# Kernel tuning notes

Hardware: AMD Instinct MI355X
Metric: run time of the kernel (lower is better)

The kernel has to match this reference:

```python
import jax, jax.numpy as jnp
import numpy as np

N_NODES = 100000
NINP = 128
N_EDGES = 1600000
EPS = 1e-12


def _gcn_conv(x, W, b, src, dst, deg_inv_sqrt):
    # PyG GCNConv: h = x W; out = D^{-1/2}(A+I)D^{-1/2} h + b
    h = x @ W  # [N, out_dim]
    norm = deg_inv_sqrt[src] * deg_inv_sqrt[dst]  # [E]
    agg = jax.ops.segment_sum(h[src] * norm[:, None], dst, num_segments=N_NODES)
    # self-loop contribution: weight deg_inv_sqrt[i]^2
    agg = agg + h * (deg_inv_sqrt ** 2)[:, None]
    return agg + b


def setup_inputs() -> dict:
    key = jax.random.key(0)
    k1, k2, k3, k4 = jax.random.split(key, 4)
    edge_index = jax.random.randint(k1, (2, N_EDGES), 0, N_NODES, dtype=jnp.int64)
    # embedding table (xavier-normal-like), padding_idx=0 row zeroed
    emb = jax.random.normal(k2, (N_NODES, NINP), dtype=jnp.float32) * (2.0 / (N_NODES + NINP)) ** 0.5
    emb = emb.at[0].set(0.0)
    W1 = jax.random.normal(k3, (NINP, 2 * NINP), dtype=jnp.float32) * (1.0 / NINP) ** 0.5
    b1 = jnp.zeros((2 * NINP,), dtype=jnp.float32)
    W2 = jax.random.normal(k4, (2 * NINP, NINP), dtype=jnp.float32) * (1.0 / (2 * NINP)) ** 0.5
    b2 = jnp.zeros((NINP,), dtype=jnp.float32)
    return {"emb": emb, "W1": W1, "b1": b1, "W2": W2, "b2": b2, "edge_index": edge_index}


def reference(emb, W1, b1, W2, b2, edge_index):
    src, dst = edge_index[0], edge_index[1]
    # symmetric GCN degree with self-loops (in-degree on dst + 1)
    deg = jax.ops.segment_sum(jnp.ones_like(dst, dtype=emb.dtype), dst, num_segments=N_NODES) + 1.0
    deg_inv_sqrt = jax.lax.rsqrt(deg)
    x = _gcn_conv(emb, W1, b1, src, dst, deg_inv_sqrt)  # [N, 2*ninp]
    # F.normalize(p=2, dim=-1)
    x = x / jnp.maximum(jnp.linalg.norm(x, axis=-1, keepdims=True), EPS)
    # dropout in eval mode (identity)
    out = _gcn_conv(x, W2, b2, src, dst, deg_inv_sqrt)  # [N, ninp]
    return out
```

## Files before the change

### kernel.cpp

```cpp
#include <hip/hip_runtime.h>
#include <hip/hip_bf16.h>

typedef __attribute__((ext_vector_type(8))) short bf16x8;
typedef __attribute__((ext_vector_type(4))) float f32x4;

#define NBUCK 391
#define BCAP 8192


__device__ __forceinline__ ushort f2bf(float f) {
    unsigned int b = __float_as_uint(f);
    unsigned int r = (b + 0x7fffu + ((b >> 16) & 1u)) >> 16;
    return (ushort)r;
}
__device__ __forceinline__ float bflo(uint v) { return __uint_as_float(v << 16); }
__device__ __forceinline__ float bfhi(uint v) { return __uint_as_float(v & 0xffff0000u); }


__global__ __launch_bounds__(256) void prep_kernel(const float* __restrict__ W1, ushort* __restrict__ W1t,
                                                   const float* __restrict__ W2, ushort* __restrict__ W2t,
                                                   int* __restrict__ gcur) {
    int b = blockIdx.x, t = threadIdx.x;
    if (b == 0) {
        if (t < NBUCK) gcur[t] = 0;
        if (t + 256 < NBUCK) gcur[t + 256] = 0;
    } else if (b <= 128) {
        int i = (b - 1) * 256 + t;
        int n = i >> 7, k = i & 127;
        W1t[i] = f2bf(W1[(size_t)k * 256 + n]);
    } else {
        int i = (b - 129) * 256 + t;
        int n = i >> 8, k = i & 255;
        W2t[i] = f2bf(W2[(size_t)k * 128 + n]);
    }
}


__global__ __launch_bounds__(256) void bucket_kernel(const int* __restrict__ src, const int* __restrict__ dst,
                                                     int* __restrict__ gcur, int2* __restrict__ pairs,
                                                     int E, int chunk) {
    __shared__ int lcnt[NBUCK];
    for (int t = threadIdx.x; t < NBUCK; t += 256) lcnt[t] = 0;
    __syncthreads();
    int e0 = blockIdx.x * chunk;
    int e1 = e0 + chunk; if (e1 > E) e1 = E;
    for (int e = e0 + (int)threadIdx.x; e < e1; e += 256)
        atomicAdd(&lcnt[dst[e] >> 8], 1);
    __syncthreads();
    for (int t = threadIdx.x; t < NBUCK; t += 256) {
        int c = lcnt[t];
        lcnt[t] = c ? atomicAdd(&gcur[t], c) : 0;
    }
    __syncthreads();
    for (int e = e0 + (int)threadIdx.x; e < e1; e += 256) {
        int d = dst[e], s = src[e];
        int b = d >> 8;
        int p = atomicAdd(&lcnt[b], 1);
        if (p < BCAP) pairs[(size_t)b * BCAP + p] = make_int2(d, s);
    }
}


__global__ __launch_bounds__(512) void scan_buckets(const int* __restrict__ gcur, int* __restrict__ bbase,
                                                    int* __restrict__ offs, int Nn, int E) {
    int i = threadIdx.x;
    int v = (i < NBUCK) ? min(gcur[i], BCAP) : 0;
    int lane = i & 63, wid = i >> 6;
    int x = v;
#pragma unroll
    for (int d = 1; d < 64; d <<= 1) {
        int y = __shfl_up(x, d, 64);
        if (lane >= d) x += y;
    }
    __shared__ int wsum[8], wpre[8];
    if (lane == 63) wsum[wid] = x;
    __syncthreads();
    if (i == 0) {
        int run = 0;
        for (int w = 0; w < 8; ++w) { wpre[w] = run; run += wsum[w]; }
        offs[Nn] = E;
    }
    __syncthreads();
    if (i < NBUCK) bbase[i] = x - v + wpre[wid];
}


__global__ __launch_bounds__(256) void csr_kernel(const int2* __restrict__ pairs, const int* __restrict__ gcur,
                                                  const int* __restrict__ bbase,
                                                  int* __restrict__ offs, float* __restrict__ dis,
                                                  int* __restrict__ csr, int Nn) {
    int b = blockIdx.x;
    int n0 = b << 8;
    int ne = min(gcur[b], BCAP);
    __shared__ int cnt[256], off[256], pos[256];
    int i = threadIdx.x;
    cnt[i] = 0;
    __syncthreads();
    const int2* pp = pairs + (size_t)b * BCAP;
    for (int e = i; e < ne; e += 256)
        atomicAdd(&cnt[pp[e].x - n0], 1);
    __syncthreads();
    int lane = i & 63, wid = i >> 6;
    int v = cnt[i];
    int x = v;
#pragma unroll
    for (int d = 1; d < 64; d <<= 1) {
        int y = __shfl_up(x, d, 64);
        if (lane >= d) x += y;
    }
    __shared__ int wsum[4], wpre[4];
    if (lane == 63) wsum[wid] = x;
    __syncthreads();
    if (i == 0) {
        int run = 0;
        for (int w = 0; w < 4; ++w) { wpre[w] = run; run += wsum[w]; }
    }
    __syncthreads();
    int excl = x - v + wpre[wid];
    off[i] = excl;
    pos[i] = 0;
    int n = n0 + i;
    if (n < Nn) {
        offs[n] = bbase[b] + excl;
        dis[n] = rsqrtf((float)v + 1.0f);
    }
    __syncthreads();
    int base = bbase[b];
    for (int e = i; e < ne; e += 256) {
        int2 r = pp[e];
        int li = r.x - n0;
        int p = atomicAdd(&pos[li], 1);
        csr[base + off[li] + p] = r.y;
    }
}


__global__ void cast_scale_kernel(const float4* __restrict__ in, const float* __restrict__ dis,
                                  ushort4* __restrict__ out, int n4) {
    int stride = gridDim.x * blockDim.x;
    for (int i = blockIdx.x * blockDim.x + threadIdx.x; i < n4; i += stride) {
        float s = dis[i >> 5];
        float4 v = in[i];
        ushort4 o;
        o.x = f2bf(v.x * s); o.y = f2bf(v.y * s); o.z = f2bf(v.z * s); o.w = f2bf(v.w * s);
        out[i] = o;
    }
}


template <bool BIAS, bool BF16OUT>
__global__ __launch_bounds__(256) void agg_kernel(const uint* __restrict__ tbl,
                                                  const int* __restrict__ offs,
                                                  const int* __restrict__ rec,
                                                  const float* __restrict__ dis,
                                                  const float* __restrict__ bias,
                                                  void* __restrict__ outp, int Nn) {
    int gw = (int)((blockIdx.x * 256 + threadIdx.x) >> 6);
    uint lane = threadIdx.x & 63;
    if (gw >= Nn) return;
    float dn = dis[gw];
    int e0 = offs[gw], e1 = offs[gw + 1];
    uint hv = tbl[(uint)gw * 64u + lane];
    float ax = bflo(hv), ay = bfhi(hv);

    for (int base = e0; base < e1; base += 16) {
        int ee = base + (int)(lane & 15u);
        uint rr = (uint)rec[ee < e1 ? ee : e1 - 1];
        uint vv[16];
#pragma unroll
        for (int j = 0; j < 16; ++j) {
            uint idx = (uint)__shfl((int)rr, j, 64);
            vv[j] = tbl[idx * 64u + lane];
        }
#pragma unroll
        for (int j = 0; j < 16; ++j) {
            uint v = (base + j < e1) ? vv[j] : 0u;
            ax += bflo(v);
            ay += bfhi(v);
        }
    }

    ax *= dn; ay *= dn;
    if (BIAS) {
        float2 bv = reinterpret_cast<const float2*>(bias)[lane];
        ax += bv.x; ay += bv.y;
    }
    if (BF16OUT) {
        reinterpret_cast<uint*>(outp)[(uint)gw * 64u + lane] =
            (uint)f2bf(ax) | ((uint)f2bf(ay) << 16);
    } else {
        float2 o; o.x = ax; o.y = ay;
        reinterpret_cast<float2*>(outp)[(uint)gw * 64u + lane] = o;
    }
}


__global__ __launch_bounds__(512, 4) void fused_gemm(const ushort* __restrict__ A,
                                                     const ushort* __restrict__ W1t,
                                                     const float* __restrict__ bias1,
                                                     const ushort* __restrict__ W2t,
                                                     const float* __restrict__ dsc,
                                                     ushort* __restrict__ out2, int M) {
    __shared__ __align__(16) ushort sA[64 * 128];
    __shared__ __align__(16) ushort xt[64 * 256];
    __shared__ float ssl[8][64];
    int tid = threadIdx.x;
    int lane = tid & 63, wid = tid >> 6;
    int g = lane >> 4, i15 = lane & 15;
    int koff = g * 8;
    int m0 = blockIdx.x * 64;

    {
        const char* Ab = reinterpret_cast<const char*>(A);
        char* sAb = reinterpret_cast<char*>(sA);
#pragma unroll
        for (int j = 0; j < 2; ++j) {
            int byte = j * 8192 + tid * 16;
            int row = byte >> 8;
            int grow = m0 + row; if (grow >= M) grow = M - 1;
            bf16x8 v = *reinterpret_cast<const bf16x8*>(Ab + (size_t)grow * 256 + (byte & 255));
            *reinterpret_cast<bf16x8*>(sAb + (byte ^ ((row & 7) << 4))) = v;
        }
    }

    bf16x8 b1f[2][4];
    float bv[2];
#pragma unroll
    for (int ns = 0; ns < 2; ++ns) {
        int c = wid * 32 + ns * 16 + i15;
        const bf16x8* p = reinterpret_cast<const bf16x8*>(W1t + (size_t)c * 128 + koff);
#pragma unroll
        for (int ks = 0; ks < 4; ++ks) b1f[ns][ks] = p[ks * 4];
        bv[ns] = bias1[c];
    }
    __syncthreads();

    const char* sAb = reinterpret_cast<const char*>(sA);
    f32x4 acc[4][2];
#pragma unroll
    for (int ms = 0; ms < 4; ++ms)
#pragma unroll
        for (int ns = 0; ns < 2; ++ns) acc[ms][ns] = (f32x4){0.f, 0.f, 0.f, 0.f};
#pragma unroll
    for (int ks = 0; ks < 4; ++ks) {
        bf16x8 a[4];
#pragma unroll
        for (int ms = 0; ms < 4; ++ms) {
            int row = ms * 16 + i15;
            int byte = row * 256 + ks * 64 + g * 16;
            a[ms] = *reinterpret_cast<const bf16x8*>(sAb + (byte ^ ((row & 7) << 4)));
        }
#pragma unroll
        for (int ms = 0; ms < 4; ++ms)
#pragma unroll
            for (int ns = 0; ns < 2; ++ns)
                acc[ms][ns] = __builtin_amdgcn_mfma_f32_16x16x32_bf16(a[ms], b1f[ns][ks], acc[ms][ns], 0, 0, 0);
    }

    float ps[4][4];
#pragma unroll
    for (int ms = 0; ms < 4; ++ms)
#pragma unroll
        for (int r = 0; r < 4; ++r) {
            float s = 0.f;
#pragma unroll
            for (int ns = 0; ns < 2; ++ns) {
                float v = acc[ms][ns][r] + bv[ns];
                acc[ms][ns][r] = v;
                s += v * v;
            }
            ps[ms][r] = s;
        }
#pragma unroll
    for (int d = 1; d < 16; d <<= 1)
#pragma unroll
        for (int ms = 0; ms < 4; ++ms)
#pragma unroll
            for (int r = 0; r < 4; ++r) ps[ms][r] += __shfl_xor(ps[ms][r], d, 64);
    if (i15 == 0) {
#pragma unroll
        for (int ms = 0; ms < 4; ++ms)
#pragma unroll
            for (int r = 0; r < 4; ++r) ssl[wid][ms * 16 + g * 4 + r] = ps[ms][r];
    }
    __syncthreads();

#pragma unroll
    for (int ms = 0; ms < 4; ++ms)
#pragma unroll
        for (int r = 0; r < 4; ++r) {
            int rt = ms * 16 + g * 4 + r;
            float tot = 0.f;
#pragma unroll
            for (int w = 0; w < 8; ++w) tot += ssl[w][rt];
            float inv = 1.0f / fmaxf(sqrtf(tot), 1e-12f);
            int sw = (rt & 7) << 3;
#pragma unroll
            for (int ns = 0; ns < 2; ++ns) {
                int col = wid * 32 + ns * 16 + i15;
                xt[(rt * 256 + col) ^ sw] = f2bf(acc[ms][ns][r] * inv);
            }
        }
    __syncthreads();

    bf16x8 b2f[8];
    {
        int c = wid * 16 + i15;
        const bf16x8* p = reinterpret_cast<const bf16x8*>(W2t + (size_t)c * 256 + koff);
#pragma unroll
        for (int ks = 0; ks < 8; ++ks) b2f[ks] = p[ks * 4];
    }

    f32x4 acc2[4];
#pragma unroll
    for (int ms = 0; ms < 4; ++ms) acc2[ms] = (f32x4){0.f, 0.f, 0.f, 0.f};
#pragma unroll
    for (int ks = 0; ks < 8; ++ks) {
        bf16x8 a2[4];
#pragma unroll
        for (int ms = 0; ms < 4; ++ms) {
            int rowA = ms * 16 + i15;
            int eb = (rowA * 256 + koff + ks * 32) ^ ((rowA & 7) << 3);
            a2[ms] = *reinterpret_cast<const bf16x8*>(&xt[eb]);
        }
#pragma unroll
        for (int ms = 0; ms < 4; ++ms)
            acc2[ms] = __builtin_amdgcn_mfma_f32_16x16x32_bf16(a2[ms], b2f[ks], acc2[ms], 0, 0, 0);
    }

#pragma unroll
    for (int ms = 0; ms < 4; ++ms)
#pragma unroll
        for (int r = 0; r < 4; ++r) {
            int row = m0 + ms * 16 + g * 4 + r;
            if (row < M) {
                float sc = dsc[row];
                out2[(size_t)row * 128 + wid * 16 + i15] = f2bf(acc2[ms][r] * sc);
            }
        }
}


extern "C" void kernel_launch(void* const* d_in, const int* in_sizes, int n_in,
                              void* d_out, int out_size, void* d_ws, size_t ws_size,
                              hipStream_t stream) {
    const float* emb = (const float*)d_in[0];
    const float* W1 = (const float*)d_in[1];
    const float* b1 = (const float*)d_in[2];
    const float* W2 = (const float*)d_in[3];
    const float* b2 = (const float*)d_in[4];
    const int* eidx = (const int*)d_in[5];

    const int Nn = in_sizes[0] / 128;
    const int E = in_sizes[5] / 2;
    const int* srcp = eidx;
    const int* dstp = eidx + E;

    float* ws = (float*)d_ws;
    size_t o = 0;
    uint* tbl1 = (uint*)(ws + o);  o += (size_t)Nn * 64;
    uint* axb = (uint*)(ws + o);   o += (size_t)Nn * 64;
    uint* tbl2 = (uint*)(ws + o);  o += (size_t)Nn * 64;
    ushort* W1t = (ushort*)(ws + o); o += 128 * 256 / 2;
    ushort* W2t = (ushort*)(ws + o); o += 256 * 128 / 2;
    float* dis = ws + o;    o += Nn;
    int* gcur = (int*)(ws + o);   o += NBUCK + 1;
    int* bbase = (int*)(ws + o);  o += NBUCK + 1;
    int* offs = (int*)(ws + o);   o += Nn + 16;
    int* csr = (int*)(ws + o);    o += E;
    int2* pairs = (int2*)(ws + o); o += (size_t)NBUCK * BCAP * 2;

    prep_kernel<<<257, 256, 0, stream>>>(W1, W1t, W2, W2t, gcur);

    int B1B = 512;
    int chunk = (E + B1B - 1) / B1B;
    bucket_kernel<<<B1B, 256, 0, stream>>>(srcp, dstp, gcur, pairs, E, chunk);
    scan_buckets<<<1, 512, 0, stream>>>(gcur, bbase, offs, Nn, E);
    csr_kernel<<<NBUCK, 256, 0, stream>>>(pairs, gcur, bbase, offs, dis, csr, Nn);

    int n4 = Nn * 128 / 4;
    cast_scale_kernel<<<2048, 256, 0, stream>>>((const float4*)emb, dis, (ushort4*)tbl1, n4);

    agg_kernel<false, true><<<(Nn + 3) / 4, 256, 0, stream>>>(tbl1, offs, csr, dis, nullptr, axb, Nn);
    fused_gemm<<<(Nn + 63) / 64, 512, 0, stream>>>((const ushort*)axb, W1t, b1, W2t, dis, (ushort*)tbl2, Nn);

    agg_kernel<true, false><<<(Nn + 3) / 4, 256, 0, stream>>>(tbl2, offs, csr, dis, b2, d_out, Nn);
}
```

Measured before the change: 234.7 us.

## Fuse prep/cast into bucket and CSR kernels; aggregate two nodes per wave

After: 233.8 us. About the same (-0.4%).

```diff
diff --git a/kernel.cpp b/kernel.cpp
--- a/kernel.cpp
+++ b/kernel.cpp
@@ -17,46 +17,42 @@
 __device__ __forceinline__ float bfhi(uint v) { return __uint_as_float(v & 0xffff0000u); }
 
 
-__global__ __launch_bounds__(256) void prep_kernel(const float* __restrict__ W1, ushort* __restrict__ W1t,
-                                                   const float* __restrict__ W2, ushort* __restrict__ W2t,
-                                                   int* __restrict__ gcur) {
-    int b = blockIdx.x, t = threadIdx.x;
-    if (b == 0) {
-        if (t < NBUCK) gcur[t] = 0;
-        if (t + 256 < NBUCK) gcur[t + 256] = 0;
-    } else if (b <= 128) {
-        int i = (b - 1) * 256 + t;
-        int n = i >> 7, k = i & 127;
-        W1t[i] = f2bf(W1[(size_t)k * 256 + n]);
-    } else {
-        int i = (b - 129) * 256 + t;
-        int n = i >> 8, k = i & 255;
-        W2t[i] = f2bf(W2[(size_t)k * 128 + n]);
-    }
-}
-
-
 __global__ __launch_bounds__(256) void bucket_kernel(const int* __restrict__ src, const int* __restrict__ dst,
                                                      int* __restrict__ gcur, int2* __restrict__ pairs,
-                                                     int E, int chunk) {
+                                                     int E, int chunk,
+                                                     const float* __restrict__ W1, ushort* __restrict__ W1t,
+                                                     const float* __restrict__ W2, ushort* __restrict__ W2t) {
+    int b = blockIdx.x, t = threadIdx.x;
+    if (b >= 512) {
+        if (b < 640) {
+            int i = (b - 512) * 256 + t;
+            int n = i >> 7, k = i & 127;
+            W1t[i] = f2bf(W1[(size_t)k * 256 + n]);
+        } else {
+            int i = (b - 640) * 256 + t;
+            int n = i >> 8, k = i & 255;
+            W2t[i] = f2bf(W2[(size_t)k * 128 + n]);
+        }
+        return;
+    }
     __shared__ int lcnt[NBUCK];
-    for (int t = threadIdx.x; t < NBUCK; t += 256) lcnt[t] = 0;
-    __syncthreads();
-    int e0 = blockIdx.x * chunk;
+    for (int q = t; q < NBUCK; q += 256) lcnt[q] = 0;
+    __syncthreads();
+    int e0 = b * chunk;
     int e1 = e0 + chunk; if (e1 > E) e1 = E;
-    for (int e = e0 + (int)threadIdx.x; e < e1; e += 256)
+    for (int e = e0 + t; e < e1; e += 256)
         atomicAdd(&lcnt[dst[e] >> 8], 1);
     __syncthreads();
-    for (int t = threadIdx.x; t < NBUCK; t += 256) {
-        int c = lcnt[t];
-        lcnt[t] = c ? atomicAdd(&gcur[t], c) : 0;
-    }
-    __syncthreads();
-    for (int e = e0 + (int)threadIdx.x; e < e1; e += 256) {
+    for (int q = t; q < NBUCK; q += 256) {
+        int c = lcnt[q];
+        lcnt[q] = c ? atomicAdd(&gcur[q], c) : 0;
+    }
+    __syncthreads();
+    for (int e = e0 + t; e < e1; e += 256) {
         int d = dst[e], s = src[e];
-        int b = d >> 8;
-        int p = atomicAdd(&lcnt[b], 1);
-        if (p < BCAP) pairs[(size_t)b * BCAP + p] = make_int2(d, s);
+        int bb = d >> 8;
+        int p = atomicAdd(&lcnt[bb], 1);
+        if (p < BCAP) pairs[(size_t)bb * BCAP + p] = make_int2(d, s);
     }
 }
 
@@ -88,11 +84,14 @@
 __global__ __launch_bounds__(256) void csr_kernel(const int2* __restrict__ pairs, const int* __restrict__ gcur,
                                                   const int* __restrict__ bbase,
                                                   int* __restrict__ offs, float* __restrict__ dis,
-                                                  int* __restrict__ csr, int Nn) {
+                                                  int* __restrict__ csr,
+                                                  const float4* __restrict__ emb4, ushort4* __restrict__ tbl4,
+                                                  int Nn) {
     int b = blockIdx.x;
     int n0 = b << 8;
     int ne = min(gcur[b], BCAP);
     __shared__ int cnt[256], off[256], pos[256];
+    __shared__ float sdis[256];
     int i = threadIdx.x;
     cnt[i] = 0;
     __syncthreads();
@@ -120,9 +119,11 @@
     off[i] = excl;
     pos[i] = 0;
     int n = n0 + i;
+    float s = rsqrtf((float)v + 1.0f);
+    sdis[i] = s;
     if (n < Nn) {
         offs[n] = bbase[b] + excl;
-        dis[n] = rsqrtf((float)v + 1.0f);
+        dis[n] = s;
     }
     __syncthreads();
     int base = bbase[b];
@@ -132,65 +133,74 @@
         int p = atomicAdd(&pos[li], 1);
         csr[base + off[li] + p] = r.y;
     }
-}
-
-
-__global__ void cast_scale_kernel(const float4* __restrict__ in, const float* __restrict__ dis,
-                                  ushort4* __restrict__ out, int n4) {
-    int stride = gridDim.x * blockDim.x;
-    for (int i = blockIdx.x * blockDim.x + threadIdx.x; i < n4; i += stride) {
-        float s = dis[i >> 5];
-        float4 v = in[i];
-        ushort4 o;
-        o.x = f2bf(v.x * s); o.y = f2bf(v.y * s); o.z = f2bf(v.z * s); o.w = f2bf(v.w * s);
-        out[i] = o;
+    for (int q = i; q < 256 * 32; q += 256) {
+        int rw = q >> 5;
+        int nn = n0 + rw;
+        if (nn < Nn) {
+            float sc = sdis[rw];
+            float4 vv = emb4[(size_t)nn * 32 + (q & 31)];
+            ushort4 o;
+            o.x = f2bf(vv.x * sc); o.y = f2bf(vv.y * sc);
+            o.z = f2bf(vv.z * sc); o.w = f2bf(vv.w * sc);
+            tbl4[(size_t)nn * 32 + (q & 31)] = o;
+        }
     }
 }
 
 
 template <bool BIAS, bool BF16OUT>
-__global__ __launch_bounds__(256) void agg_kernel(const uint* __restrict__ tbl,
-                                                  const int* __restrict__ offs,
-                                                  const int* __restrict__ rec,
-                                                  const float* __restrict__ dis,
-                                                  const float* __restrict__ bias,
-                                                  void* __restrict__ outp, int Nn) {
-    int gw = (int)((blockIdx.x * 256 + threadIdx.x) >> 6);
-    uint lane = threadIdx.x & 63;
-    if (gw >= Nn) return;
-    float dn = dis[gw];
-    int e0 = offs[gw], e1 = offs[gw + 1];
-    uint hv = tbl[(uint)gw * 64u + lane];
-    float ax = bflo(hv), ay = bfhi(hv);
-
-    for (int base = e0; base < e1; base += 16) {
-        int ee = base + (int)(lane & 15u);
-        uint rr = (uint)rec[ee < e1 ? ee : e1 - 1];
-        uint vv[16];
-#pragma unroll
-        for (int j = 0; j < 16; ++j) {
-            uint idx = (uint)__shfl((int)rr, j, 64);
-            vv[j] = tbl[idx * 64u + lane];
-        }
-#pragma unroll
-        for (int j = 0; j < 16; ++j) {
-            uint v = (base + j < e1) ? vv[j] : 0u;
-            ax += bflo(v);
-            ay += bfhi(v);
-        }
-    }
-
-    ax *= dn; ay *= dn;
+__global__ __launch_bounds__(256) void agg2x(const uint2* __restrict__ tbl2x,
+                                             const int* __restrict__ offs,
+                                             const int* __restrict__ rec,
+                                             const float* __restrict__ dis,
+                                             const float* __restrict__ bias,
+                                             void* __restrict__ outp, int Nn) {
+    int wave = (int)((blockIdx.x * 256 + threadIdx.x) >> 6);
+    int lane = threadIdx.x & 63;
+    int i31 = lane & 31;
+    int gw = wave * 2 + (lane >> 5);
+    bool valid = gw < Nn;
+    int gc = valid ? gw : Nn - 1;
+    float dn = dis[gc];
+    int e0 = offs[gc], e1 = offs[gc + 1];
+    int eclamp = (e1 > 0) ? e1 - 1 : 0;
+    uint2 hv = tbl2x[(size_t)gc * 32 + i31];
+    float a0 = bflo(hv.x), a1 = bfhi(hv.x), a2 = bflo(hv.y), a3 = bfhi(hv.y);
+
+    for (int base = e0; __any(base < e1); base += 8) {
+        int ee = base + (i31 & 7);
+        uint rr = (uint)rec[ee < e1 ? ee : eclamp];
+        uint ix[8];
+#pragma unroll
+        for (int j = 0; j < 8; ++j) ix[j] = (uint)__shfl((int)rr, j, 32);
+        uint2 vv[8];
+#pragma unroll
+        for (int j = 0; j < 8; ++j) vv[j] = tbl2x[(size_t)ix[j] * 32u + (uint)i31];
+#pragma unroll
+        for (int j = 0; j < 8; ++j) {
+            bool ok = (base + j) < e1;
+            uint xx = ok ? vv[j].x : 0u;
+            uint yy = ok ? vv[j].y : 0u;
+            a0 += bflo(xx); a1 += bfhi(xx);
+            a2 += bflo(yy); a3 += bfhi(yy);
+        }
+    }
+
+    a0 *= dn; a1 *= dn; a2 *= dn; a3 *= dn;
     if (BIAS) {
-        float2 bv = reinterpret_cast<const float2*>(bias)[lane];
-        ax += bv.x; ay += bv.y;
-    }
-    if (BF16OUT) {
-        reinterpret_cast<uint*>(outp)[(uint)gw * 64u + lane] =
-            (uint)f2bf(ax) | ((uint)f2bf(ay) << 16);
-    } else {
-        float2 o; o.x = ax; o.y = ay;
-        reinterpret_cast<float2*>(outp)[(uint)gw * 64u + lane] = o;
+        float4 bv = reinterpret_cast<const float4*>(bias)[i31];
+        a0 += bv.x; a1 += bv.y; a2 += bv.z; a3 += bv.w;
+    }
+    if (valid) {
+        if (BF16OUT) {
+            uint2 o;
+            o.x = (uint)f2bf(a0) | ((uint)f2bf(a1) << 16);
+            o.y = (uint)f2bf(a2) | ((uint)f2bf(a3) << 16);
+            reinterpret_cast<uint2*>(outp)[(size_t)gw * 32 + i31] = o;
+        } else {
+            float4 o = make_float4(a0, a1, a2, a3);
+            reinterpret_cast<float4*>(outp)[(size_t)gw * 32 + i31] = o;
+        }
     }
 }
 
@@ -370,19 +380,17 @@
     int* csr = (int*)(ws + o);    o += E;
     int2* pairs = (int2*)(ws + o); o += (size_t)NBUCK * BCAP * 2;
 
-    prep_kernel<<<257, 256, 0, stream>>>(W1, W1t, W2, W2t, gcur);
+    hipMemsetAsync(gcur, 0, (NBUCK + 1) * sizeof(int), stream);
 
     int B1B = 512;
     int chunk = (E + B1B - 1) / B1B;
-    bucket_kernel<<<B1B, 256, 0, stream>>>(srcp, dstp, gcur, pairs, E, chunk);
+    bucket_kernel<<<768, 256, 0, stream>>>(srcp, dstp, gcur, pairs, E, chunk, W1, W1t, W2, W2t);
     scan_buckets<<<1, 512, 0, stream>>>(gcur, bbase, offs, Nn, E);
-    csr_kernel<<<NBUCK, 256, 0, stream>>>(pairs, gcur, bbase, offs, dis, csr, Nn);
-
-    int n4 = Nn * 128 / 4;
-    cast_scale_kernel<<<2048, 256, 0, stream>>>((const float4*)emb, dis, (ushort4*)tbl1, n4);
-
-    agg_kernel<false, true><<<(Nn + 3) / 4, 256, 0, stream>>>(tbl1, offs, csr, dis, nullptr, axb, Nn);
+    csr_kernel<<<NBUCK, 256, 0, stream>>>(pairs, gcur, bbase, offs, dis, csr,
+                                          (const float4*)emb, (ushort4*)tbl1, Nn);
+
+    agg2x<false, true><<<(Nn + 7) / 8, 256, 0, stream>>>((const uint2*)tbl1, offs, csr, dis, nullptr, axb, Nn);
     fused_gemm<<<(Nn + 63) / 64, 512, 0, stream>>>((const ushort*)axb, W1t, b1, W2t, dis, (ushort*)tbl2, Nn);
 
-    agg_kernel<true, false><<<(Nn + 3) / 4, 256, 0, stream>>>(tbl2, offs, csr, dis, b2, d_out, Nn);
-}
+    agg2x<true, false><<<(Nn + 7) / 8, 256, 0, stream>>>((const uint2*)tbl2, offs, csr, dis, b2, d_out, Nn);
+}
```
